# Optimization experiments

Measured on AMD Instinct MI355X. Metric: run time of the kernel, lower is better.

The kernel has to match this reference:

```python
import jax, jax.numpy as jnp
import numpy as np

N_NODES = 50000
N_EDGES = 1600000
D_IN = 128
D_HID = 128


def setup_inputs() -> dict:
    key = jax.random.key(0)
    ks = jax.random.split(key, 6)
    edge_index = jax.random.randint(ks[0], (2, N_EDGES), 0, N_NODES, dtype=jnp.int32)
    emb = jax.random.normal(ks[1], (N_NODES, D_IN), dtype=jnp.float32) * 0.1
    W1 = jax.random.normal(ks[2], (D_IN, D_HID), dtype=jnp.float32) * (1.0 / np.sqrt(D_IN))
    b1 = jnp.zeros((D_HID,), dtype=jnp.float32)
    W2 = jax.random.normal(ks[3], (D_HID, D_HID), dtype=jnp.float32) * (1.0 / np.sqrt(D_HID))
    b2 = jnp.zeros((D_HID,), dtype=jnp.float32)
    head_w = jax.random.normal(ks[4], (D_HID, 1), dtype=jnp.float32) * (1.0 / np.sqrt(D_HID))
    head_b = jnp.zeros((1,), dtype=jnp.float32)
    return {"edge_index": edge_index, "emb": emb, "W1": W1, "b1": b1,
            "W2": W2, "b2": b2, "head_w": head_w, "head_b": head_b}


def _gcn_norm(edge_index, num_nodes):
    # PyG GCNConv default: add self-loops, sym-normalize D^-1/2 (A+I) D^-1/2.
    loops = jnp.arange(num_nodes, dtype=edge_index.dtype)
    src = jnp.concatenate([edge_index[0], loops])  # [E+N]
    dst = jnp.concatenate([edge_index[1], loops])  # [E+N]
    deg = jax.ops.segment_sum(jnp.ones_like(dst, dtype=jnp.float32), dst,
                              num_segments=num_nodes)  # [N], >=1 via self-loops
    dis = jax.lax.rsqrt(deg)
    norm = dis[src] * dis[dst]  # [E+N]
    return src, dst, norm


def _gcn_conv(x, W, b, src, dst, norm, num_nodes):
    h = x @ W                                  # [N, D] dense transform first
    msg = h[src] * norm[:, None]               # [E+N, D] gather + scale
    out = jax.ops.segment_sum(msg, dst, num_segments=num_nodes)  # scatter-add
    return out + b


def reference(edge_index, emb, W1, b1, W2, b2, head_w, head_b):
    src, dst, norm = _gcn_norm(edge_index, N_NODES)
    x = jax.nn.relu(_gcn_conv(emb, W1, b1, src, dst, norm, N_NODES))
    x = jax.nn.relu(_gcn_conv(x, W2, b2, src, dst, norm, N_NODES))
    scores = jax.nn.sigmoid(x @ head_w + head_b)[:, 0]  # [N]
    return scores
```

## Files before the change

### kernel.cpp

```cpp
#include <hip/hip_runtime.h>
#include <hip/hip_fp16.h>
#include <math.h>

#define D 128
#define D4 32
#define AP 136
#define AP8 144
#define NBUCK 512
#define NT 512
#define EPB 2048
#define BCAP2 4096

typedef _Float16 f16x8 __attribute__((ext_vector_type(8)));
typedef float f32x4 __attribute__((ext_vector_type(4)));
typedef float f32x2 __attribute__((ext_vector_type(2)));


__global__ void prep_all_kernel(const float* __restrict__ W1, _Float16* __restrict__ Wt1,
                                const float* __restrict__ W2, _Float16* __restrict__ Wt2,
                                int* __restrict__ bcnt) {
    int t = threadIdx.x;
    if (blockIdx.x == 0) { bcnt[t] = 0; bcnt[256 + t] = 0; }
    int half = blockIdx.x & 63;
    const float* W = (blockIdx.x < 64) ? W1 : W2;
    _Float16* Wt   = (blockIdx.x < 64) ? Wt1 : Wt2;
    int i = half * 256 + t;
    int k = i >> 7, c = i & 127;
    Wt[c * 128 + k] = (_Float16)W[i];
}


__global__ __launch_bounds__(NT) void bucket_pass1(const int* __restrict__ src,
                                                   const int* __restrict__ dst,
                                                   int* __restrict__ bcnt,
                                                   unsigned* __restrict__ buckets,
                                                   int E, unsigned magicM) {
    __shared__ unsigned stage[EPB];
    __shared__ int lcnt[NBUCK], loff[NBUCK], gbase[NBUCK];

    int t = threadIdx.x;
    int base = blockIdx.x * EPB;
    int nblk = min(EPB, E - base);
    lcnt[t] = 0;
    __syncthreads();

    for (int i = t; i < nblk; i += NT) {
        unsigned d = (unsigned)dst[base + i];
        int b = (int)(((unsigned long long)d * magicM) >> 24);
        atomicAdd(&lcnt[b], 1);
    }
    __syncthreads();

    int v = lcnt[t];
    loff[t] = v;
    __syncthreads();
    for (int off = 1; off < NT; off <<= 1) {
        int x = (t >= off) ? loff[t - off] : 0;
        __syncthreads();
        loff[t] += x;
        __syncthreads();
    }
    int incl = loff[t];
    __syncthreads();
    loff[t] = incl - v;
    gbase[t] = atomicAdd(&bcnt[t], v);
    lcnt[t] = 0;
    __syncthreads();

    for (int i = t; i < nblk; i += NT) {
        unsigned s = (unsigned)src[base + i];
        unsigned d = (unsigned)dst[base + i];
        unsigned pk = (s << 16) | d;
        int b = (int)(((unsigned long long)d * magicM) >> 24);
        int p = atomicAdd(&lcnt[b], 1);
        stage[loff[b] + p] = pk;
    }
    __syncthreads();

    for (int i = t; i < nblk; i += NT) {
        unsigned pk = stage[i];
        int b = (int)(((unsigned long long)(pk & 0xffffu) * magicM) >> 24);
        int pos = gbase[b] + (i - loff[b]);
        if (pos < BCAP2) buckets[(size_t)b * BCAP2 + pos] = pk;
    }
}

__global__ __launch_bounds__(NT) void csr_pass2(const unsigned* __restrict__ buckets,
                                                const int* __restrict__ bcnt,
                                                int* __restrict__ row_ptr,
                                                int* __restrict__ row_mid,
                                                float* __restrict__ dis,
                                                unsigned short* __restrict__ col,
                                                int N, int npb, int E, int mid) {
    __shared__ int cnt[NT], cntA[NT], sc[NT], excl[NT], curA[NT], curB[NT];
    __shared__ unsigned short estage[BCAP2];

    int b = blockIdx.x;
    int t = threadIdx.x;

    int bv = min(bcnt[t], BCAP2);
    sc[t] = bv;
    __syncthreads();
    for (int off = 1; off < NT; off <<= 1) {
        int x = (t >= off) ? sc[t - off] : 0;
        __syncthreads();
        sc[t] += x;
        __syncthreads();
    }
    int base = sc[b] - min(bcnt[b], BCAP2);
    if (b == 0 && t == 0) row_ptr[N] = E;
    __syncthreads();

    int lo = b * npb;
    int nn = min(npb, N - lo);
    int n = min(bcnt[b], BCAP2);
    const unsigned* bk = buckets + (size_t)b * BCAP2;

    cnt[t] = 0;
    cntA[t] = 0;
    __syncthreads();
    for (int i = t; i < n; i += NT) {
        unsigned pk = bk[i];
        int dl = (int)(pk & 0xffffu) - lo;
        atomicAdd(&cnt[dl], 1);
        if ((int)(pk >> 16) < mid) atomicAdd(&cntA[dl], 1);
    }
    __syncthreads();
    int v = cnt[t];
    sc[t] = v;
    __syncthreads();
    for (int off = 1; off < NT; off <<= 1) {
        int x = (t >= off) ? sc[t - off] : 0;
        __syncthreads();
        sc[t] += x;
        __syncthreads();
    }
    excl[t] = sc[t] - v;
    if (t < nn) {
        row_ptr[lo + t] = base + excl[t];
        row_mid[lo + t] = base + excl[t] + cntA[t];
        dis[lo + t] = rsqrtf((float)v + 1.0f);
    }
    curA[t] = 0;
    curB[t] = 0;
    __syncthreads();
    for (int i = t; i < n; i += NT) {
        unsigned pk = bk[i];
        int dl = (int)(pk & 0xffffu) - lo;
        int s = (int)(pk >> 16);
        int p;
        if (s < mid) p = excl[dl] + atomicAdd(&curA[dl], 1);
        else         p = excl[dl] + cntA[dl] + atomicAdd(&curB[dl], 1);
        estage[p] = (unsigned short)s;
    }
    __syncthreads();
    for (int i = t; i < n; i += NT) col[base + i] = estage[i];
}


#define GEMM_CORE                                                            \
    const uint4* Wt16 = (const uint4*)Wt;                                    \
    for (int i = t; i < 128 * 16; i += 256) {                                \
        int r = i >> 4, ch = i & 15;                                         \
        *(uint4*)&Ws[r * AP + ch * 8] = Wt16[i];                             \
    }                                                                        \
    __syncthreads();                                                         \
    int wave = t >> 6;                                                       \
    int lane = t & 63;                                                       \
    int m16 = lane & 15;                                                     \
    int quad = lane >> 4;                                                    \
    f32x4 acc[8];                                                            \
    for (int n = 0; n < 8; n++) acc[n] = (f32x4){0.f, 0.f, 0.f, 0.f};        \
    _Pragma("unroll")                                                        \
    for (int kc = 0; kc < 4; kc++) {                                         \
        f16x8 a = *(const f16x8*)&As[(wave * 16 + m16) * AP + kc * 32 + quad * 8]; \
        _Pragma("unroll")                                                    \
        for (int n = 0; n < 8; n++) {                                        \
            f16x8 bfrag = *(const f16x8*)&Ws[(n * 16 + m16) * AP + kc * 32 + quad * 8]; \
            acc[n] = __builtin_amdgcn_mfma_f32_16x16x32_f16(a, bfrag, acc[n], 0, 0, 0); \
        }                                                                    \
    }                                                                        \
    __syncthreads();                                                         \
    unsigned char* Cs8 = (unsigned char*)As;                                 \
    float dv[4];                                                             \
    _Pragma("unroll")                                                        \
    for (int r = 0; r < 4; r++) {                                            \
        int grow = row0 + wave * 16 + quad * 4 + r;                          \
        dv[r] = (grow < N) ? dis[grow] : 0.f;                                \
    }                                                                        \
    _Pragma("unroll")                                                        \
    for (int n = 0; n < 8; n++)                                              \
        _Pragma("unroll")                                                    \
        for (int r = 0; r < 4; r++) {                                        \
            float val = acc[n][r] * dv[r];                                   \
            int wq = __builtin_amdgcn_cvt_pk_fp8_f32(val, val, 0, false);    \
            Cs8[(wave * 16 + quad * 4 + r) * AP8 + n * 16 + m16] = (unsigned char)(wq & 0xff); \
        }                                                                    \
    __syncthreads();                                                         \
    uint4* C16 = (uint4*)C8;                                                 \
    for (int i = lane; i < 128; i += 64) {                                   \
        int r = i >> 3, ch = i & 7;                                          \
        int grow = row0 + wave * 16 + r;                                     \
        if (grow < N)                                                        \
            C16[(size_t)grow * 8 + ch] = *(const uint4*)&Cs8[(wave * 16 + r) * AP8 + ch * 16]; \
    }

__global__ __launch_bounds__(256) void gemm_f32a_fp8c(const float* __restrict__ A,
                                                      const _Float16* __restrict__ Wt,
                                                      const float* __restrict__ dis,
                                                      unsigned int* __restrict__ C8, int N) {
    __shared__ _Float16 As[64 * AP];
    __shared__ _Float16 Ws[128 * AP];
    int t = threadIdx.x;
    int row0 = blockIdx.x * 64;
    const float4* A4 = (const float4*)A;
    for (int i = t; i < 64 * 16; i += 256) {
        int r = i >> 4, ch = i & 15;
        uint4 v = make_uint4(0, 0, 0, 0);
        if (row0 + r < N) {
            float4 a0 = A4[(size_t)(row0 + r) * 32 + ch * 2];
            float4 a1 = A4[(size_t)(row0 + r) * 32 + ch * 2 + 1];
            __half2 h0 = __floats2half2_rn(a0.x, a0.y);
            __half2 h1 = __floats2half2_rn(a0.z, a0.w);
            __half2 h2 = __floats2half2_rn(a1.x, a1.y);
            __half2 h3 = __floats2half2_rn(a1.z, a1.w);
            v.x = *(unsigned*)&h0; v.y = *(unsigned*)&h1;
            v.z = *(unsigned*)&h2; v.w = *(unsigned*)&h3;
        }
        *(uint4*)&As[r * AP + ch * 8] = v;
    }
    GEMM_CORE
}

__global__ __launch_bounds__(256) void gemm_f16a_fp8c(const _Float16* __restrict__ A,
                                                      const _Float16* __restrict__ Wt,
                                                      const float* __restrict__ dis,
                                                      unsigned int* __restrict__ C8, int N) {
    __shared__ _Float16 As[64 * AP];
    __shared__ _Float16 Ws[128 * AP];
    int t = threadIdx.x;
    int row0 = blockIdx.x * 64;
    const uint4* A16 = (const uint4*)A;
    for (int i = t; i < 64 * 16; i += 256) {
        int r = i >> 4, ch = i & 15;
        uint4 v = make_uint4(0, 0, 0, 0);
        if (row0 + r < N) v = A16[(size_t)(row0 + r) * 16 + ch];
        *(uint4*)&As[r * AP + ch * 8] = v;
    }
    GEMM_CORE
}


__device__ __forceinline__ void acc8(float4& a, unsigned int u) {
    f32x2 lo = __builtin_amdgcn_cvt_pk_f32_fp8((int)u, false);
    f32x2 hi = __builtin_amdgcn_cvt_pk_f32_fp8((int)u, true);
    a.x += lo[0]; a.y += lo[1]; a.z += hi[0]; a.w += hi[1];
}

#define AGG_RANGE(lo_, hi_)                                                     \
    for (int base = (lo_); base < (hi_); base += 32) {                          \
        int cnt = min(32, (hi_) - base);                                        \
        int myc = (base + lane < (hi_)) ? (int)col[base + lane] : 0;            \
        int j = 0;                                                              \
        for (; j + 8 <= cnt; j += 8) {                                          \
            int s0 = __shfl(myc, j + 0, 32); int s1 = __shfl(myc, j + 1, 32);   \
            int s2 = __shfl(myc, j + 2, 32); int s3 = __shfl(myc, j + 3, 32);   \
            int s4 = __shfl(myc, j + 4, 32); int s5 = __shfl(myc, j + 5, 32);   \
            int s6 = __shfl(myc, j + 6, 32); int s7 = __shfl(myc, j + 7, 32);   \
            unsigned int u0 = t8[(size_t)s0 * D4 + lane];                       \
            unsigned int u1 = t8[(size_t)s1 * D4 + lane];                       \
            unsigned int u2 = t8[(size_t)s2 * D4 + lane];                       \
            unsigned int u3 = t8[(size_t)s3 * D4 + lane];                       \
            unsigned int u4 = t8[(size_t)s4 * D4 + lane];                       \
            unsigned int u5 = t8[(size_t)s5 * D4 + lane];                       \
            unsigned int u6 = t8[(size_t)s6 * D4 + lane];                       \
            unsigned int u7 = t8[(size_t)s7 * D4 + lane];                       \
            acc8(acc, u0); acc8(acc, u1); acc8(acc, u2); acc8(acc, u3);         \
            acc8(acc, u4); acc8(acc, u5); acc8(acc, u6); acc8(acc, u7);         \
        }                                                                       \
        for (; j < cnt; j++) {                                                  \
            int s = __shfl(myc, j, 32);                                         \
            acc8(acc, t8[(size_t)s * D4 + lane]);                               \
        }                                                                       \
    }

#define AGG8_BODY                                                               \
    float4 acc = make_float4(0.f, 0.f, 0.f, 0.f);                               \
    acc8(acc, t8[(size_t)node * D4 + lane]);        \
    int e0 = row_ptr[node], e1 = row_ptr[node + 1];                             \
    int em = row_mid[node];                                                     \
    AGG_RANGE(e0, em)                \
    AGG_RANGE(em, e1)               \
    float di = dis[node];                                                       \
    float4 bb = ((const float4*)bias)[lane];                                    \
    float4 o;                                                                   \
    o.x = fmaxf(fmaf(di, acc.x, bb.x), 0.f);                                    \
    o.y = fmaxf(fmaf(di, acc.y, bb.y), 0.f);                                    \
    o.z = fmaxf(fmaf(di, acc.z, bb.z), 0.f);                                    \
    o.w = fmaxf(fmaf(di, acc.w, bb.w), 0.f);

__global__ void agg_fp8_kernel(const unsigned int* __restrict__ t8, const float* __restrict__ bias,
                               const int* __restrict__ row_ptr, const int* __restrict__ row_mid,
                               const unsigned short* __restrict__ col,
                               const float* __restrict__ dis, _Float16* __restrict__ xout, int N) {
    int t = threadIdx.x;
    int node = blockIdx.x * 8 + (t >> 5);
    int lane = t & 31;
    if (node >= N) return;
    AGG8_BODY
    __half2 q0 = __floats2half2_rn(o.x, o.y);
    __half2 q1 = __floats2half2_rn(o.z, o.w);
    uint2 u;
    u.x = *(unsigned int*)&q0;
    u.y = *(unsigned int*)&q1;
    ((uint2*)xout)[(size_t)node * D4 + lane] = u;
}

__global__ void agg_head_fp8_kernel(const unsigned int* __restrict__ t8, const float* __restrict__ bias,
                                    const int* __restrict__ row_ptr, const int* __restrict__ row_mid,
                                    const unsigned short* __restrict__ col,
                                    const float* __restrict__ dis,
                                    const float* __restrict__ head_w, const float* __restrict__ head_b,
                                    float* __restrict__ out, int N) {
    int t = threadIdx.x;
    int node = blockIdx.x * 8 + (t >> 5);
    int lane = t & 31;
    if (node >= N) return;
    AGG8_BODY
    float4 wv = ((const float4*)head_w)[lane];
    float s = o.x * wv.x + o.y * wv.y + o.z * wv.z + o.w * wv.w;
    for (int m = 1; m < 32; m <<= 1) s += __shfl_xor(s, m, 64);
    if (lane == 0) {
        float v = s + head_b[0];
        out[node] = 1.0f / (1.0f + expf(-v));
    }
}


extern "C" void kernel_launch(void* const* d_in, const int* in_sizes, int n_in,
                              void* d_out, int out_size, void* d_ws, size_t ws_size,
                              hipStream_t stream) {
    const int*   edge   = (const int*)d_in[0];
    const float* emb    = (const float*)d_in[1];
    const float* W1     = (const float*)d_in[2];
    const float* b1     = (const float*)d_in[3];
    const float* W2     = (const float*)d_in[4];
    const float* b2     = (const float*)d_in[5];
    const float* head_w = (const float*)d_in[6];
    const float* head_b = (const float*)d_in[7];
    float* out = (float*)d_out;

    int E = in_sizes[0] / 2;
    int N = in_sizes[1] / D;
    const int* srcp = edge;
    const int* dstp = edge + E;

    char* w = (char*)d_ws;
    auto alloc = [&](size_t bytes) -> char* {
        char* p = w;
        w += (bytes + 15) & ~(size_t)15;
        return p;
    };
    unsigned int*   t8      = (unsigned int*)alloc((size_t)N * D);
    _Float16*       x1h     = (_Float16*)alloc((size_t)N * D * 2);
    unsigned*       buckets = (unsigned*)alloc((size_t)NBUCK * BCAP2 * 4);
    _Float16*       Wt1     = (_Float16*)alloc((size_t)D * D * 2);
    _Float16*       Wt2     = (_Float16*)alloc((size_t)D * D * 2);
    unsigned short* col     = (unsigned short*)alloc((size_t)E * 2);
    int*            bcnt    = (int*)alloc(NBUCK * 4);
    int*            row_ptr = (int*)alloc((size_t)(N + 1) * 4);
    int*            row_mid = (int*)alloc((size_t)N * 4);
    float*          dis     = (float*)alloc((size_t)N * 4);

    int npb = (N + NBUCK - 1) / NBUCK;
    unsigned magicM = (16777216u + (unsigned)npb - 1) / (unsigned)npb;
    int mid = N / 2;
    int gP1 = (E + EPB - 1) / EPB;
    int gG = (N + 63) / 64;
    int gA = (N + 7) / 8;

    prep_all_kernel<<<128, 256, 0, stream>>>(W1, Wt1, W2, Wt2, bcnt);
    bucket_pass1<<<gP1, NT, 0, stream>>>(srcp, dstp, bcnt, buckets, E, magicM);
    csr_pass2<<<NBUCK, NT, 0, stream>>>(buckets, bcnt, row_ptr, row_mid, dis, col, N, npb, E, mid);

    gemm_f32a_fp8c<<<gG, 256, 0, stream>>>(emb, Wt1, dis, t8, N);
    agg_fp8_kernel<<<gA, 256, 0, stream>>>(t8, b1, row_ptr, row_mid, col, dis, x1h, N);
    gemm_f16a_fp8c<<<gG, 256, 0, stream>>>(x1h, Wt2, dis, t8, N);
    agg_head_fp8_kernel<<<gA, 256, 0, stream>>>(t8, b2, row_ptr, row_mid, col, dis,
                                                head_w, head_b, out, N);
}
```

Before: 209.2 us.

## Split aggregation into two grid-synced phases over source halves via cooperative launch

The two aggregation kernels are replaced by cooperative kernels, one block per resident slot across the whole GPU. Each node's edges are split by source index into a lower and an upper half. All blocks first gather from the lower half of the feature table, keep partial sums in shared memory, grid-sync, then gather from the upper half, so each phase's gather working set is about half the table and fits better in cache. The edge-per-block constant for bucketing is doubled, and csr_pass2 reuses the cnt array in place of curA. The price is a grid-wide barrier, a static occupancy check with a fallback to the old kernels, and an assumed count of 256 CUs.

```diff
diff --git a/kernel.cpp b/kernel.cpp
--- a/kernel.cpp
+++ b/kernel.cpp
@@ -1,6 +1,9 @@
 #include <hip/hip_runtime.h>
+#include <hip/hip_cooperative_groups.h>
 #include <hip/hip_fp16.h>
 #include <math.h>
+
+namespace cg = cooperative_groups;
 
 #define D 128
 #define D4 32
@@ -8,8 +11,12 @@
 #define AP8 144
 #define NBUCK 512
 #define NT 512
-#define EPB 2048
+#define EPB 4096
 #define BCAP2 4096
+
+#define CU_COUNT 256
+#define COOP_BPCU 8
+#define COOP_BLOCKS (CU_COUNT * COOP_BPCU)
 
 typedef _Float16 f16x8 __attribute__((ext_vector_type(8)));
 typedef float f32x4 __attribute__((ext_vector_type(4)));
@@ -92,7 +99,7 @@
                                                 float* __restrict__ dis,
                                                 unsigned short* __restrict__ col,
                                                 int N, int npb, int E, int mid) {
-    __shared__ int cnt[NT], cntA[NT], sc[NT], excl[NT], curA[NT], curB[NT];
+    __shared__ int cnt[NT], cntA[NT], sc[NT], excl[NT], curB[NT];
     __shared__ unsigned short estage[BCAP2];
 
     int b = blockIdx.x;
@@ -141,7 +148,7 @@
         row_mid[lo + t] = base + excl[t] + cntA[t];
         dis[lo + t] = rsqrtf((float)v + 1.0f);
     }
-    curA[t] = 0;
+    cnt[t] = 0;
     curB[t] = 0;
     __syncthreads();
     for (int i = t; i < n; i += NT) {
@@ -149,7 +156,7 @@
         int dl = (int)(pk & 0xffffu) - lo;
         int s = (int)(pk >> 16);
         int p;
-        if (s < mid) p = excl[dl] + atomicAdd(&curA[dl], 1);
+        if (s < mid) p = excl[dl] + atomicAdd(&cnt[dl], 1);
         else         p = excl[dl] + cntA[dl] + atomicAdd(&curB[dl], 1);
         estage[p] = (unsigned short)s;
     }
@@ -284,13 +291,7 @@
         }                                                                       \
     }
 
-#define AGG8_BODY                                                               \
-    float4 acc = make_float4(0.f, 0.f, 0.f, 0.f);                               \
-    acc8(acc, t8[(size_t)node * D4 + lane]);        \
-    int e0 = row_ptr[node], e1 = row_ptr[node + 1];                             \
-    int em = row_mid[node];                                                     \
-    AGG_RANGE(e0, em)                \
-    AGG_RANGE(em, e1)               \
+#define AGG_EPILOGUE                                                            \
     float di = dis[node];                                                       \
     float4 bb = ((const float4*)bias)[lane];                                    \
     float4 o;                                                                   \
@@ -299,26 +300,120 @@
     o.z = fmaxf(fmaf(di, acc.z, bb.z), 0.f);                                    \
     o.w = fmaxf(fmaf(di, acc.w, bb.w), 0.f);
 
+#define HEAD_EPILOGUE                                                           \
+    float4 wv = ((const float4*)head_w)[lane];                                  \
+    float s = o.x * wv.x + o.y * wv.y + o.z * wv.z + o.w * wv.w;                \
+    for (int m = 1; m < 32; m <<= 1) s += __shfl_xor(s, m, 64);                 \
+    if (lane == 0) {                                                            \
+        float v = s + head_b[0];                                                \
+        out[node] = 1.0f / (1.0f + expf(-v));                                   \
+    }
+
+#define X1_PACK_WRITE                                                           \
+    __half2 q0 = __floats2half2_rn(o.x, o.y);                                   \
+    __half2 q1 = __floats2half2_rn(o.z, o.w);                                   \
+    uint2 u;                                                                    \
+    u.x = *(unsigned int*)&q0;                                                  \
+    u.y = *(unsigned int*)&q1;                                                  \
+    ((uint2*)xout)[(size_t)node * D4 + lane] = u;
+
+
+__global__ __launch_bounds__(256, 8) void agg1_coop(const unsigned int* __restrict__ t8,
+                                                    const float* __restrict__ bias,
+                                                    const int* __restrict__ row_ptr,
+                                                    const int* __restrict__ row_mid,
+                                                    const unsigned short* __restrict__ col,
+                                                    const float* __restrict__ dis,
+                                                    _Float16* __restrict__ xout,
+                                                    int N, int npb, int mid) {
+    __shared__ float4 accs[1024];
+    cg::grid_group gg = cg::this_grid();
+    int t = threadIdx.x, slot = t >> 5, lane = t & 31;
+    int nb = blockIdx.x * npb;
+    int ngroups = (npb + 7) >> 3;
+    for (int g = 0; g < ngroups; ++g) {
+        int ln = g * 8 + slot;
+        int node = nb + ln;
+        float4 acc = make_float4(0.f, 0.f, 0.f, 0.f);
+        if (ln < npb && node < N) {
+            if (node < mid) acc8(acc, t8[(size_t)node * D4 + lane]);
+            int e0 = row_ptr[node], em = row_mid[node];
+            AGG_RANGE(e0, em)
+        }
+        accs[ln * 32 + lane] = acc;
+    }
+    gg.sync();
+    for (int g = 0; g < ngroups; ++g) {
+        int ln = g * 8 + slot;
+        int node = nb + ln;
+        if (ln >= npb || node >= N) continue;
+        float4 acc = accs[ln * 32 + lane];
+        if (node >= mid) acc8(acc, t8[(size_t)node * D4 + lane]);
+        int em = row_mid[node], e1 = row_ptr[node + 1];
+        AGG_RANGE(em, e1)
+        AGG_EPILOGUE
+        X1_PACK_WRITE
+    }
+}
+
+__global__ __launch_bounds__(256, 8) void agg_head_coop(const unsigned int* __restrict__ t8,
+                                                        const float* __restrict__ bias,
+                                                        const int* __restrict__ row_ptr,
+                                                        const int* __restrict__ row_mid,
+                                                        const unsigned short* __restrict__ col,
+                                                        const float* __restrict__ dis,
+                                                        const float* __restrict__ head_w,
+                                                        const float* __restrict__ head_b,
+                                                        float* __restrict__ out,
+                                                        int N, int npb, int mid) {
+    __shared__ float4 accs[1024];
+    cg::grid_group gg = cg::this_grid();
+    int t = threadIdx.x, slot = t >> 5, lane = t & 31;
+    int nb = blockIdx.x * npb;
+    int ngroups = (npb + 7) >> 3;
+    for (int g = 0; g < ngroups; ++g) {
+        int ln = g * 8 + slot;
+        int node = nb + ln;
+        float4 acc = make_float4(0.f, 0.f, 0.f, 0.f);
+        if (ln < npb && node < N) {
+            if (node < mid) acc8(acc, t8[(size_t)node * D4 + lane]);
+            int e0 = row_ptr[node], em = row_mid[node];
+            AGG_RANGE(e0, em)
+        }
+        accs[ln * 32 + lane] = acc;
+    }
+    gg.sync();
+    for (int g = 0; g < ngroups; ++g) {
+        int ln = g * 8 + slot;
+        int node = nb + ln;
+        if (ln >= npb || node >= N) continue;
+        float4 acc = accs[ln * 32 + lane];
+        if (node >= mid) acc8(acc, t8[(size_t)node * D4 + lane]);
+        int em = row_mid[node], e1 = row_ptr[node + 1];
+        AGG_RANGE(em, e1)
+        AGG_EPILOGUE
+        HEAD_EPILOGUE
+    }
+}
+
+
 __global__ void agg_fp8_kernel(const unsigned int* __restrict__ t8, const float* __restrict__ bias,
-                               const int* __restrict__ row_ptr, const int* __restrict__ row_mid,
-                               const unsigned short* __restrict__ col,
+                               const int* __restrict__ row_ptr, const unsigned short* __restrict__ col,
                                const float* __restrict__ dis, _Float16* __restrict__ xout, int N) {
     int t = threadIdx.x;
     int node = blockIdx.x * 8 + (t >> 5);
     int lane = t & 31;
     if (node >= N) return;
-    AGG8_BODY
-    __half2 q0 = __floats2half2_rn(o.x, o.y);
-    __half2 q1 = __floats2half2_rn(o.z, o.w);
-    uint2 u;
-    u.x = *(unsigned int*)&q0;
-    u.y = *(unsigned int*)&q1;
-    ((uint2*)xout)[(size_t)node * D4 + lane] = u;
+    float4 acc = make_float4(0.f, 0.f, 0.f, 0.f);
+    acc8(acc, t8[(size_t)node * D4 + lane]);
+    int e0 = row_ptr[node], e1 = row_ptr[node + 1];
+    AGG_RANGE(e0, e1)
+    AGG_EPILOGUE
+    X1_PACK_WRITE
 }
 
 __global__ void agg_head_fp8_kernel(const unsigned int* __restrict__ t8, const float* __restrict__ bias,
-                                    const int* __restrict__ row_ptr, const int* __restrict__ row_mid,
-                                    const unsigned short* __restrict__ col,
+                                    const int* __restrict__ row_ptr, const unsigned short* __restrict__ col,
                                     const float* __restrict__ dis,
                                     const float* __restrict__ head_w, const float* __restrict__ head_b,
                                     float* __restrict__ out, int N) {
@@ -326,14 +421,12 @@
     int node = blockIdx.x * 8 + (t >> 5);
     int lane = t & 31;
     if (node >= N) return;
-    AGG8_BODY
-    float4 wv = ((const float4*)head_w)[lane];
-    float s = o.x * wv.x + o.y * wv.y + o.z * wv.z + o.w * wv.w;
-    for (int m = 1; m < 32; m <<= 1) s += __shfl_xor(s, m, 64);
-    if (lane == 0) {
-        float v = s + head_b[0];
-        out[node] = 1.0f / (1.0f + expf(-v));
-    }
+    float4 acc = make_float4(0.f, 0.f, 0.f, 0.f);
+    acc8(acc, t8[(size_t)node * D4 + lane]);
+    int e0 = row_ptr[node], e1 = row_ptr[node + 1];
+    AGG_RANGE(e0, e1)
+    AGG_EPILOGUE
+    HEAD_EPILOGUE
 }
 
 
@@ -378,14 +471,45 @@
     int gP1 = (E + EPB - 1) / EPB;
     int gG = (N + 63) / 64;
     int gA = (N + 7) / 8;
+    int cnpb = (N + COOP_BLOCKS - 1) / COOP_BLOCKS;
+
+    static int coop_ok = -1;
+    if (coop_ok < 0) {
+        int mb1 = 0, mb2 = 0;
+        hipError_t q1 = hipOccupancyMaxActiveBlocksPerMultiprocessor(&mb1, agg1_coop, 256, 0);
+        hipError_t q2 = hipOccupancyMaxActiveBlocksPerMultiprocessor(&mb2, agg_head_coop, 256, 0);
+        coop_ok = (q1 == hipSuccess && q2 == hipSuccess &&
+                   mb1 >= COOP_BPCU && mb2 >= COOP_BPCU) ? 1 : 0;
+    }
+    bool use_coop = (coop_ok == 1) && (cnpb <= 32);
 
     prep_all_kernel<<<128, 256, 0, stream>>>(W1, Wt1, W2, Wt2, bcnt);
     bucket_pass1<<<gP1, NT, 0, stream>>>(srcp, dstp, bcnt, buckets, E, magicM);
     csr_pass2<<<NBUCK, NT, 0, stream>>>(buckets, bcnt, row_ptr, row_mid, dis, col, N, npb, E, mid);
 
     gemm_f32a_fp8c<<<gG, 256, 0, stream>>>(emb, Wt1, dis, t8, N);
-    agg_fp8_kernel<<<gA, 256, 0, stream>>>(t8, b1, row_ptr, row_mid, col, dis, x1h, N);
+
+    bool launched1 = false;
+    if (use_coop) {
+        void* a1[] = {(void*)&t8, (void*)&b1, (void*)&row_ptr, (void*)&row_mid,
+                      (void*)&col, (void*)&dis, (void*)&x1h, (void*)&N, (void*)&cnpb, (void*)&mid};
+        launched1 = (hipLaunchCooperativeKernel(agg1_coop, dim3(COOP_BLOCKS), dim3(256),
+                                                a1, 0, stream) == hipSuccess);
+    }
+    if (!launched1)
+        agg_fp8_kernel<<<gA, 256, 0, stream>>>(t8, b1, row_ptr, col, dis, x1h, N);
+
     gemm_f16a_fp8c<<<gG, 256, 0, stream>>>(x1h, Wt2, dis, t8, N);
-    agg_head_fp8_kernel<<<gA, 256, 0, stream>>>(t8, b2, row_ptr, row_mid, col, dis,
-                                                head_w, head_b, out, N);
-}
+
+    bool launched2 = false;
+    if (use_coop && launched1) {
+        void* a2[] = {(void*)&t8, (void*)&b2, (void*)&row_ptr, (void*)&row_mid,
+                      (void*)&col, (void*)&dis, (void*)&head_w, (void*)&head_b,
+                      (void*)&out, (void*)&N, (void*)&cnpb, (void*)&mid};
+        launched2 = (hipLaunchCooperativeKernel(agg_head_coop, dim3(COOP_BLOCKS), dim3(256),
+                                                a2, 0, stream) == hipSuccess);
+    }
+    if (!launched2)
+        agg_head_fp8_kernel<<<gA, 256, 0, stream>>>(t8, b2, row_ptr, col, dis,
+                                                    head_w, head_b, out, N);
+}
```

Result: faster. 197.6 us (-5.6%).

## Split aggregation into two source-half phases with fp32 partial-sum buffer

Applied to the files above, without the earlier changes.

Each aggregation is split into two kernels: phase A gathers only source nodes below mid, phase B gathers the upper half and applies the epilogue. Each pass then touches only half of the fp8 feature table, so the gathered working set may fit in cache better. In exchange it writes and reads an N×128 fp32 partial buffer (about 25 MB each way) and adds kernel launches. Edges per block in pass 1 are doubled, and the csr_pass2 shared-memory counter curA is replaced by reusing cnt.

```diff
diff --git a/kernel.cpp b/kernel.cpp
--- a/kernel.cpp
+++ b/kernel.cpp
@@ -8,7 +8,7 @@
 #define AP8 144
 #define NBUCK 512
 #define NT 512
-#define EPB 2048
+#define EPB 4096
 #define BCAP2 4096
 
 typedef _Float16 f16x8 __attribute__((ext_vector_type(8)));
@@ -92,7 +92,7 @@
                                                 float* __restrict__ dis,
                                                 unsigned short* __restrict__ col,
                                                 int N, int npb, int E, int mid) {
-    __shared__ int cnt[NT], cntA[NT], sc[NT], excl[NT], curA[NT], curB[NT];
+    __shared__ int cnt[NT], cntA[NT], sc[NT], excl[NT], curB[NT];
     __shared__ unsigned short estage[BCAP2];
 
     int b = blockIdx.x;
@@ -141,7 +141,7 @@
         row_mid[lo + t] = base + excl[t] + cntA[t];
         dis[lo + t] = rsqrtf((float)v + 1.0f);
     }
-    curA[t] = 0;
+    cnt[t] = 0;
     curB[t] = 0;
     __syncthreads();
     for (int i = t; i < n; i += NT) {
@@ -149,7 +149,7 @@
         int dl = (int)(pk & 0xffffu) - lo;
         int s = (int)(pk >> 16);
         int p;
-        if (s < mid) p = excl[dl] + atomicAdd(&curA[dl], 1);
+        if (s < mid) p = excl[dl] + atomicAdd(&cnt[dl], 1);
         else         p = excl[dl] + cntA[dl] + atomicAdd(&curB[dl], 1);
         estage[p] = (unsigned short)s;
     }
@@ -284,13 +284,7 @@
         }                                                                       \
     }
 
-#define AGG8_BODY                                                               \
-    float4 acc = make_float4(0.f, 0.f, 0.f, 0.f);                               \
-    acc8(acc, t8[(size_t)node * D4 + lane]);        \
-    int e0 = row_ptr[node], e1 = row_ptr[node + 1];                             \
-    int em = row_mid[node];                                                     \
-    AGG_RANGE(e0, em)                \
-    AGG_RANGE(em, e1)               \
+#define AGG_EPILOGUE                                                            \
     float di = dis[node];                                                       \
     float4 bb = ((const float4*)bias)[lane];                                    \
     float4 o;                                                                   \
@@ -299,15 +293,38 @@
     o.z = fmaxf(fmaf(di, acc.z, bb.z), 0.f);                                    \
     o.w = fmaxf(fmaf(di, acc.w, bb.w), 0.f);
 
-__global__ void agg_fp8_kernel(const unsigned int* __restrict__ t8, const float* __restrict__ bias,
-                               const int* __restrict__ row_ptr, const int* __restrict__ row_mid,
-                               const unsigned short* __restrict__ col,
-                               const float* __restrict__ dis, _Float16* __restrict__ xout, int N) {
+__global__ void agg_phaseA(const unsigned int* __restrict__ t8,
+                           const int* __restrict__ row_ptr,
+                           const int* __restrict__ row_mid,
+                           const unsigned short* __restrict__ col,
+                           float* __restrict__ pacc, int N, int mid) {
     int t = threadIdx.x;
     int node = blockIdx.x * 8 + (t >> 5);
     int lane = t & 31;
     if (node >= N) return;
-    AGG8_BODY
+    float4 acc = make_float4(0.f, 0.f, 0.f, 0.f);
+    if (node < mid) acc8(acc, t8[(size_t)node * D4 + lane]);
+    int e0 = row_ptr[node], em = row_mid[node];
+    AGG_RANGE(e0, em)
+    f32x4 pv = {acc.x, acc.y, acc.z, acc.w};
+    __builtin_nontemporal_store(pv, (f32x4*)pacc + (size_t)node * 32 + lane);
+}
+
+__global__ void agg1_phaseB(const unsigned int* __restrict__ t8, const float* __restrict__ bias,
+                            const int* __restrict__ row_ptr, const int* __restrict__ row_mid,
+                            const unsigned short* __restrict__ col,
+                            const float* __restrict__ dis, const float* __restrict__ pacc,
+                            _Float16* __restrict__ xout, int N, int mid) {
+    int t = threadIdx.x;
+    int node = blockIdx.x * 8 + (t >> 5);
+    int lane = t & 31;
+    if (node >= N) return;
+    f32x4 pv = __builtin_nontemporal_load((const f32x4*)pacc + (size_t)node * 32 + lane);
+    float4 acc = make_float4(pv[0], pv[1], pv[2], pv[3]);
+    if (node >= mid) acc8(acc, t8[(size_t)node * D4 + lane]);
+    int em = row_mid[node], e1 = row_ptr[node + 1];
+    AGG_RANGE(em, e1)
+    AGG_EPILOGUE
     __half2 q0 = __floats2half2_rn(o.x, o.y);
     __half2 q1 = __floats2half2_rn(o.z, o.w);
     uint2 u;
@@ -316,17 +333,22 @@
     ((uint2*)xout)[(size_t)node * D4 + lane] = u;
 }
 
-__global__ void agg_head_fp8_kernel(const unsigned int* __restrict__ t8, const float* __restrict__ bias,
-                                    const int* __restrict__ row_ptr, const int* __restrict__ row_mid,
-                                    const unsigned short* __restrict__ col,
-                                    const float* __restrict__ dis,
-                                    const float* __restrict__ head_w, const float* __restrict__ head_b,
-                                    float* __restrict__ out, int N) {
+__global__ void agg_head_phaseB(const unsigned int* __restrict__ t8, const float* __restrict__ bias,
+                                const int* __restrict__ row_ptr, const int* __restrict__ row_mid,
+                                const unsigned short* __restrict__ col,
+                                const float* __restrict__ dis, const float* __restrict__ pacc,
+                                const float* __restrict__ head_w, const float* __restrict__ head_b,
+                                float* __restrict__ out, int N, int mid) {
     int t = threadIdx.x;
     int node = blockIdx.x * 8 + (t >> 5);
     int lane = t & 31;
     if (node >= N) return;
-    AGG8_BODY
+    f32x4 pv = __builtin_nontemporal_load((const f32x4*)pacc + (size_t)node * 32 + lane);
+    float4 acc = make_float4(pv[0], pv[1], pv[2], pv[3]);
+    if (node >= mid) acc8(acc, t8[(size_t)node * D4 + lane]);
+    int em = row_mid[node], e1 = row_ptr[node + 1];
+    AGG_RANGE(em, e1)
+    AGG_EPILOGUE
     float4 wv = ((const float4*)head_w)[lane];
     float s = o.x * wv.x + o.y * wv.y + o.z * wv.z + o.w * wv.w;
     for (int m = 1; m < 32; m <<= 1) s += __shfl_xor(s, m, 64);
@@ -363,6 +385,7 @@
     };
     unsigned int*   t8      = (unsigned int*)alloc((size_t)N * D);
     _Float16*       x1h     = (_Float16*)alloc((size_t)N * D * 2);
+    float*          pacc    = (float*)alloc((size_t)N * D * 4);
     unsigned*       buckets = (unsigned*)alloc((size_t)NBUCK * BCAP2 * 4);
     _Float16*       Wt1     = (_Float16*)alloc((size_t)D * D * 2);
     _Float16*       Wt2     = (_Float16*)alloc((size_t)D * D * 2);
@@ -384,8 +407,10 @@
     csr_pass2<<<NBUCK, NT, 0, stream>>>(buckets, bcnt, row_ptr, row_mid, dis, col, N, npb, E, mid);
 
     gemm_f32a_fp8c<<<gG, 256, 0, stream>>>(emb, Wt1, dis, t8, N);
-    agg_fp8_kernel<<<gA, 256, 0, stream>>>(t8, b1, row_ptr, row_mid, col, dis, x1h, N);
+    agg_phaseA<<<gA, 256, 0, stream>>>(t8, row_ptr, row_mid, col, pacc, N, mid);
+    agg1_phaseB<<<gA, 256, 0, stream>>>(t8, b1, row_ptr, row_mid, col, dis, pacc, x1h, N, mid);
     gemm_f16a_fp8c<<<gG, 256, 0, stream>>>(x1h, Wt2, dis, t8, N);
-    agg_head_fp8_kernel<<<gA, 256, 0, stream>>>(t8, b2, row_ptr, row_mid, col, dis,
-                                                head_w, head_b, out, N);
-}
+    agg_phaseA<<<gA, 256, 0, stream>>>(t8, row_ptr, row_mid, col, pacc, N, mid);
+    agg_head_phaseB<<<gA, 256, 0, stream>>>(t8, b2, row_ptr, row_mid, col, dis, pacc,
+                                            head_w, head_b, out, N, mid);
+}
```

Result: slower. 215.2 us (+2.9%).
